# Kernel tuning notes

Hardware: AMD Instinct MI355X
Metric: run time of the kernel (lower is better)

Reference implementation:

```python
import jax, jax.numpy as jnp
import numpy as np

N_NODES = 100000
FT_IN = 128
NHID = 64
N_EDGES = 1000000


def setup_inputs() -> dict:
    key = jax.random.key(0)
    ks = jax.random.split(key, 9)
    seq = jax.random.normal(ks[0], (N_NODES, FT_IN), dtype=jnp.float32)
    row = jax.random.randint(ks[1], (N_EDGES,), 0, N_NODES, dtype=jnp.int32)
    col = jax.random.randint(ks[2], (N_EDGES,), 0, N_NODES, dtype=jnp.int32)
    # encoder: LogReg Linear(ft_in, nhid), xavier-uniform weight, zero bias
    lim_enc = float(np.sqrt(6.0 / (FT_IN + NHID)))
    W_enc = jax.random.uniform(ks[3], (NHID, FT_IN), jnp.float32, -lim_enc, lim_enc)
    b_enc = jnp.zeros((NHID,), jnp.float32)
    # decoder lin1: Linear(2*nhid, nhid)
    lim1 = float(1.0 / np.sqrt(2 * NHID))
    W1 = jax.random.uniform(ks[4], (NHID, 2 * NHID), jnp.float32, -lim1, lim1)
    b1 = jax.random.uniform(ks[5], (NHID,), jnp.float32, -lim1, lim1)
    # decoder lin2: Linear(nhid, 1)
    lim2 = float(1.0 / np.sqrt(NHID))
    W2 = jax.random.uniform(ks[6], (1, NHID), jnp.float32, -lim2, lim2)
    b2 = jax.random.uniform(ks[7], (1,), jnp.float32, -lim2, lim2)
    return {"seq": seq, "W_enc": W_enc, "b_enc": b_enc, "W1": W1, "b1": b1,
            "W2": W2, "b2": b2, "row": row, "col": col}


def reference(seq, W_enc, b_enc, W1, b1, W2, b2, row, col):
    # encoder: z_all = seq @ W_enc^T + b_enc   -> [N, nhid]
    z = seq @ W_enc.T + b_enc
    # edge gather + concat -> [E, 2*nhid]
    e = jnp.concatenate([z[row], z[col]], axis=-1)
    h = jax.nn.relu(e @ W1.T + b1)             # [E, nhid]
    out = h @ W2.T + b2                        # [E, 1]
    return out.reshape(-1)
```

## Files before the change

### kernel.cpp

```cpp
#include <hip/hip_runtime.h>
#include <hip/hip_bf16.h>


#define K_IN  128
#define N_OUT 128
#define LDA   136
#define LDB   136

typedef short bf16x8 __attribute__((ext_vector_type(8)));
typedef float f32x4  __attribute__((ext_vector_type(4)));
typedef _Float16 half8 __attribute__((ext_vector_type(8)));

static __device__ __forceinline__ short f2bf(float x) {
    __hip_bfloat16 h = __float2bfloat16(x);
    return *reinterpret_cast<short*>(&h);
}

__global__ __launch_bounds__(256) void prep_kernel(
        const float* __restrict__ W_enc, const float* __restrict__ b_enc,
        const float* __restrict__ W1,    const float* __restrict__ b1,
        __hip_bfloat16* __restrict__ Wb, float* __restrict__ bcat)
{
    int idx = blockIdx.x * blockDim.x + threadIdx.x;
    if (idx >= N_OUT * K_IN) return;
    int i = idx >> 7;
    int k = idx & 127;
    int irow = i & 63;
    int joff = (i < 64) ? 0 : 64;
    float s = 0.f;
    #pragma unroll 8
    for (int j = 0; j < 64; ++j)
        s = fmaf(W1[irow * 128 + joff + j], W_enc[j * 128 + k], s);
    Wb[i * K_IN + k] = __float2bfloat16(s);
    if (k == 0) {
        float b = 0.f;
        for (int j = 0; j < 64; ++j)
            b = fmaf(W1[irow * 128 + joff + j], b_enc[j], b);
        if (i < 64) b += b1[i];
        bcat[i] = b;
    }
}

__global__ __launch_bounds__(256) void node_proj_kernel(
        const float* __restrict__ seq, const __hip_bfloat16* __restrict__ Wb,
        const float* __restrict__ bcat, _Float16* __restrict__ UVh, int nNodes)
{
    __shared__ short As[64 * LDA];
    __shared__ short Bs[N_OUT * LDB];

    int tid  = threadIdx.x;
    int base = blockIdx.x * 64;

    #pragma unroll
    for (int it = 0; it < 8; ++it) {
        int f4 = tid + 256 * it;
        int r  = f4 >> 5;
        int cb = (f4 & 31) * 4;
        int node = base + r;
        if (node >= nNodes) node = nNodes - 1;
        float4 s = *(const float4*)(seq + (size_t)node * K_IN + cb);
        short4 p;
        p.x = f2bf(s.x); p.y = f2bf(s.y); p.z = f2bf(s.z); p.w = f2bf(s.w);
        *(short4*)(As + r * LDA + cb) = p;
    }
    #pragma unroll
    for (int it = 0; it < 8; ++it) {
        int c8 = tid + 256 * it;
        int r  = c8 >> 4;
        int cb = (c8 & 15) * 8;
        int4 w = *(const int4*)(Wb + r * K_IN + cb);
        *(int4*)(Bs + r * LDB + cb) = w;
    }
    __syncthreads();

    int lane = tid & 63;
    int w    = tid >> 6;
    int lr   = lane & 15;
    int lg   = lane >> 4;

    f32x4 acc[8];
    #pragma unroll
    for (int nt = 0; nt < 8; ++nt) {
        float b = bcat[nt * 16 + lr];
        acc[nt] = (f32x4){b, b, b, b};
    }

    #pragma unroll
    for (int kk = 0; kk < 4; ++kk) {
        bf16x8 a = *(bf16x8*)(As + (16 * w + lr) * LDA + kk * 32 + lg * 8);
        #pragma unroll
        for (int nt = 0; nt < 8; ++nt) {
            bf16x8 b = *(bf16x8*)(Bs + (nt * 16 + lr) * LDB + kk * 32 + lg * 8);
            acc[nt] = __builtin_amdgcn_mfma_f32_16x16x32_bf16(a, b, acc[nt], 0, 0, 0);
        }
    }

    int nodeb = base + 16 * w + lg * 4;
    #pragma unroll
    for (int j = 0; j < 4; ++j) {
        int node = nodeb + j;
        if (node < nNodes) {
            #pragma unroll
            for (int nt = 0; nt < 8; ++nt)
                UVh[(size_t)node * N_OUT + nt * 16 + lr] = (_Float16)acc[nt][j];
        }
    }
}

__global__ __launch_bounds__(256) void edge_kernel(
        const _Float16* __restrict__ UVh, const int* __restrict__ row,
        const int* __restrict__ col, const float* __restrict__ W2,
        const float* __restrict__ b2, float* __restrict__ out, int nEdges)
{
    int l = threadIdx.x & 7;
    float w2v[8];
    #pragma unroll
    for (int j = 0; j < 8; ++j) w2v[j] = W2[l * 8 + j];
    float bb = b2[0];

    int gid = (int)((blockIdx.x * blockDim.x + threadIdx.x) >> 3);
    int ng  = (int)((gridDim.x * blockDim.x) >> 3);

    for (int e = gid; e < nEdges; e += ng) {
        int r = row[e];
        int c = col[e];
        half8 a = *(const half8*)(UVh + (size_t)r * N_OUT + l * 8);
        half8 b = *(const half8*)(UVh + (size_t)c * N_OUT + 64 + l * 8);
        float p = 0.f;
        #pragma unroll
        for (int j = 0; j < 8; ++j) {
            float h = (float)a[j] + (float)b[j];
            h = fmaxf(h, 0.f);
            p = fmaf(h, w2v[j], p);
        }
        p += __shfl_xor(p, 1);
        p += __shfl_xor(p, 2);
        p += __shfl_xor(p, 4);
        if (l == 0) out[e] = p + bb;
    }
}

extern "C" void kernel_launch(void* const* d_in, const int* in_sizes, int n_in,
                              void* d_out, int out_size, void* d_ws, size_t ws_size,
                              hipStream_t stream) {
    const float* seq   = (const float*)d_in[0];
    const float* W_enc = (const float*)d_in[1];
    const float* b_enc = (const float*)d_in[2];
    const float* W1    = (const float*)d_in[3];
    const float* b1    = (const float*)d_in[4];
    const float* W2    = (const float*)d_in[5];
    const float* b2    = (const float*)d_in[6];
    const int*   row   = (const int*)d_in[7];
    const int*   col   = (const int*)d_in[8];
    float* out = (float*)d_out;

    int nNodes = in_sizes[0] / K_IN;
    int nEdges = in_sizes[7];

    _Float16* UVh = (_Float16*)d_ws;
    __hip_bfloat16* Wb = (__hip_bfloat16*)((char*)d_ws +
                         (size_t)nNodes * N_OUT * sizeof(_Float16));
    float* bcat = (float*)((char*)Wb + N_OUT * K_IN * sizeof(__hip_bfloat16));

    prep_kernel<<<(N_OUT * K_IN + 255) / 256, 256, 0, stream>>>(
        W_enc, b_enc, W1, b1, Wb, bcat);

    int nblocksA = (nNodes + 63) / 64;
    node_proj_kernel<<<nblocksA, 256, 0, stream>>>(seq, Wb, bcat, UVh, nNodes);

    edge_kernel<<<2048, 256, 0, stream>>>(UVh, row, col, W2, b2, out, nEdges);
}
```

Measured before the change: 60.02 us.

## Load node-projection A operand directly from global; batch four edges per group

The node projection kernel no longer stages seq rows through shared memory. Each lane loads its MFMA A fragment straight from global memory and converts it to bf16 in registers, which removes the As buffer and its LDS traffic and frees LDS for occupancy. The edge kernel now handles four edges per 8-lane group, using vectorized int4 index loads, eight independent gathers in flight and one float4 store, to raise memory-level parallelism. The cost is more registers in the edge kernel and less coalesced global A loads in the projection.

```diff
diff --git a/kernel.cpp b/kernel.cpp
--- a/kernel.cpp
+++ b/kernel.cpp
@@ -4,7 +4,6 @@
 
 #define K_IN  128
 #define N_OUT 128
-#define LDA   136
 #define LDB   136
 
 typedef short bf16x8 __attribute__((ext_vector_type(8)));
@@ -45,7 +44,6 @@
         const float* __restrict__ seq, const __hip_bfloat16* __restrict__ Wb,
         const float* __restrict__ bcat, _Float16* __restrict__ UVh, int nNodes)
 {
-    __shared__ short As[64 * LDA];
     __shared__ short Bs[N_OUT * LDB];
 
     int tid  = threadIdx.x;
@@ -53,23 +51,10 @@
 
     #pragma unroll
     for (int it = 0; it < 8; ++it) {
-        int f4 = tid + 256 * it;
-        int r  = f4 >> 5;
-        int cb = (f4 & 31) * 4;
-        int node = base + r;
-        if (node >= nNodes) node = nNodes - 1;
-        float4 s = *(const float4*)(seq + (size_t)node * K_IN + cb);
-        short4 p;
-        p.x = f2bf(s.x); p.y = f2bf(s.y); p.z = f2bf(s.z); p.w = f2bf(s.w);
-        *(short4*)(As + r * LDA + cb) = p;
-    }
-    #pragma unroll
-    for (int it = 0; it < 8; ++it) {
         int c8 = tid + 256 * it;
         int r  = c8 >> 4;
         int cb = (c8 & 15) * 8;
-        int4 w = *(const int4*)(Wb + r * K_IN + cb);
-        *(int4*)(Bs + r * LDB + cb) = w;
+        *(int4*)(Bs + r * LDB + cb) = *(const int4*)(Wb + r * K_IN + cb);
     }
     __syncthreads();
 
@@ -77,6 +62,10 @@
     int w    = tid >> 6;
     int lr   = lane & 15;
     int lg   = lane >> 4;
+
+    int arow = base + 16 * w + lr;
+    if (arow >= nNodes) arow = nNodes - 1;
+    const float* aptr = seq + (size_t)arow * K_IN + lg * 8;
 
     f32x4 acc[8];
     #pragma unroll
@@ -87,7 +76,11 @@
 
     #pragma unroll
     for (int kk = 0; kk < 4; ++kk) {
-        bf16x8 a = *(bf16x8*)(As + (16 * w + lr) * LDA + kk * 32 + lg * 8);
+        float4 f0 = *(const float4*)(aptr + kk * 32);
+        float4 f1 = *(const float4*)(aptr + kk * 32 + 4);
+        bf16x8 a;
+        a[0] = f2bf(f0.x); a[1] = f2bf(f0.y); a[2] = f2bf(f0.z); a[3] = f2bf(f0.w);
+        a[4] = f2bf(f1.x); a[5] = f2bf(f1.y); a[6] = f2bf(f1.z); a[7] = f2bf(f1.w);
         #pragma unroll
         for (int nt = 0; nt < 8; ++nt) {
             bf16x8 b = *(bf16x8*)(Bs + (nt * 16 + lr) * LDB + kk * 32 + lg * 8);
@@ -121,22 +114,51 @@
     int gid = (int)((blockIdx.x * blockDim.x + threadIdx.x) >> 3);
     int ng  = (int)((gridDim.x * blockDim.x) >> 3);
 
-    for (int e = gid; e < nEdges; e += ng) {
-        int r = row[e];
-        int c = col[e];
-        half8 a = *(const half8*)(UVh + (size_t)r * N_OUT + l * 8);
-        half8 b = *(const half8*)(UVh + (size_t)c * N_OUT + 64 + l * 8);
-        float p = 0.f;
-        #pragma unroll
-        for (int j = 0; j < 8; ++j) {
-            float h = (float)a[j] + (float)b[j];
-            h = fmaxf(h, 0.f);
-            p = fmaf(h, w2v[j], p);
+    for (int e0 = gid * 4; e0 < nEdges; e0 += ng * 4) {
+        if (e0 + 4 <= nEdges) {
+            int4 r4 = *(const int4*)(row + e0);
+            int4 c4 = *(const int4*)(col + e0);
+            half8 a0 = *(const half8*)(UVh + (size_t)r4.x * N_OUT + l * 8);
+            half8 b0 = *(const half8*)(UVh + (size_t)c4.x * N_OUT + 64 + l * 8);
+            half8 a1 = *(const half8*)(UVh + (size_t)r4.y * N_OUT + l * 8);
+            half8 b1 = *(const half8*)(UVh + (size_t)c4.y * N_OUT + 64 + l * 8);
+            half8 a2 = *(const half8*)(UVh + (size_t)r4.z * N_OUT + l * 8);
+            half8 b2v = *(const half8*)(UVh + (size_t)c4.z * N_OUT + 64 + l * 8);
+            half8 a3 = *(const half8*)(UVh + (size_t)r4.w * N_OUT + l * 8);
+            half8 b3 = *(const half8*)(UVh + (size_t)c4.w * N_OUT + 64 + l * 8);
+
+            float p0 = 0.f, p1 = 0.f, p2 = 0.f, p3 = 0.f;
+            #pragma unroll
+            for (int j = 0; j < 8; ++j) {
+                p0 = fmaf(fmaxf((float)a0[j] + (float)b0[j], 0.f), w2v[j], p0);
+                p1 = fmaf(fmaxf((float)a1[j] + (float)b1[j], 0.f), w2v[j], p1);
+                p2 = fmaf(fmaxf((float)a2[j] + (float)b2v[j], 0.f), w2v[j], p2);
+                p3 = fmaf(fmaxf((float)a3[j] + (float)b3[j], 0.f), w2v[j], p3);
+            }
+            #pragma unroll
+            for (int s = 1; s < 8; s <<= 1) {
+                p0 += __shfl_xor(p0, s);
+                p1 += __shfl_xor(p1, s);
+                p2 += __shfl_xor(p2, s);
+                p3 += __shfl_xor(p3, s);
+            }
+            if (l == 0)
+                *(float4*)(out + e0) = make_float4(p0 + bb, p1 + bb, p2 + bb, p3 + bb);
+        } else {
+            for (int e = e0; e < nEdges; ++e) {
+                int r = row[e];
+                int c = col[e];
+                half8 a = *(const half8*)(UVh + (size_t)r * N_OUT + l * 8);
+                half8 b = *(const half8*)(UVh + (size_t)c * N_OUT + 64 + l * 8);
+                float p = 0.f;
+                #pragma unroll
+                for (int j = 0; j < 8; ++j)
+                    p = fmaf(fmaxf((float)a[j] + (float)b[j], 0.f), w2v[j], p);
+                #pragma unroll
+                for (int s = 1; s < 8; s <<= 1) p += __shfl_xor(p, s);
+                if (l == 0) out[e] = p + bb;
+            }
         }
-        p += __shfl_xor(p, 1);
-        p += __shfl_xor(p, 2);
-        p += __shfl_xor(p, 4);
-        if (l == 0) out[e] = p + bb;
     }
 }
 
```

Measured after the change: 59.85 us. No clear change (-0.3%).
